# Optimization experiments

Measured on AMD Instinct MI355X. Metric: run time of the kernel, lower is better.

Reference implementation:

```python
import jax, jax.numpy as jnp
import numpy as np

N_NODES = 50000
EPS_NORM = 1e-12
EPS_ENT = 1e-8

def _l2norm(x):
    # torch.nn.functional.normalize: x / clamp(||x||, min=1e-12)
    n = jnp.sqrt(jnp.sum(x * x, axis=-1, keepdims=True))
    return x / jnp.maximum(n, EPS_NORM)

def _layer(hidden, src, dst, edge_type, multi_emb, proto_emb):
    # hidden: [N,H]; multi_emb: [R,P,H]; proto_emb: [P,H]
    inp_j = hidden[src]                          # [E,H] gather
    rel_basis = multi_emb[edge_type]             # [E,P,H] gather
    sims = jnp.einsum('eh,ph->ep', _l2norm(inp_j), _l2norm(proto_emb))  # cosine sim [E,P]
    proto_proba = jax.nn.softmax(sims, axis=1)   # [E,P]
    msg = jnp.einsum('ep,eph->eh', proto_proba, rel_basis)              # [E,H]
    ent = -jnp.sum(proto_proba * jnp.log(proto_proba + EPS_ENT), axis=1)  # [E]
    logits = -ent
    # scatter_softmax over destination index
    seg_max = jax.ops.segment_max(logits, dst, num_segments=N_NODES)
    ex = jnp.exp(logits - seg_max[dst])
    denom = jax.ops.segment_sum(ex, dst, num_segments=N_NODES)
    attn = ex / denom[dst]                       # [E]
    out = jax.ops.segment_sum(attn[:, None] * msg, dst, num_segments=N_NODES)  # [N,H]
    return out

def setup_inputs() -> dict:
    key = jax.random.key(0)
    ks = jax.random.split(key, 6)
    E = 800000
    H, R, P, L = 128, 18, 18, 3  # num_layers=4 -> 3 NBFCluttr layers
    edge_index = jax.random.randint(ks[0], (2, E), 0, N_NODES, dtype=jnp.int64) if jax.config.read('jax_enable_x64') else jax.random.randint(ks[0], (2, E), 0, N_NODES, dtype=jnp.int32)
    edge_type = jax.random.randint(ks[1], (E,), 0, R, dtype=edge_index.dtype)
    tail_indices = jax.random.randint(ks[2], (1024,), 0, N_NODES, dtype=edge_index.dtype)
    multi_embeddings = jax.random.uniform(ks[3], (L, R, P, H), dtype=jnp.float32)
    proto_embeddings = jax.random.uniform(ks[4], (L, P, H), dtype=jnp.float32)
    source_embedding = jax.random.uniform(ks[5], (H,), dtype=jnp.float32)
    return {"edge_index": edge_index, "edge_type": edge_type, "tail_indices": tail_indices,
            "multi_embeddings": multi_embeddings, "proto_embeddings": proto_embeddings,
            "source_embedding": source_embedding}

def reference(edge_index, edge_type, tail_indices, multi_embeddings, proto_embeddings, source_embedding):
    src, dst = edge_index[0], edge_index[1]
    H = source_embedding.shape[0]
    # boundary condition: source node gets source_embedding, rest zero
    hidden = jnp.zeros((N_NODES, H), dtype=source_embedding.dtype).at[0].set(source_embedding)
    L = multi_embeddings.shape[0]
    for l in range(L):  # small fixed loop over structurally distinct layers
        hidden = _layer(hidden, src, dst, edge_type, multi_embeddings[l], proto_embeddings[l])
    # apply_classifier, eval_mode=True, use_mlp_classifier=False -> cosine sims to last layer prototypes
    out_emb = hidden[tail_indices]               # [B,H]
    sims = jnp.einsum('nh,ph->np', _l2norm(out_emb), _l2norm(proto_embeddings[-1]))
    return sims  # gumbel_softmax_sample with eval_mode=True returns logits unchanged
```

## Files before the change

### kernel.cpp

```cpp
#include <hip/hip_runtime.h>
#include <hip/hip_bf16.h>


#define N_NODES 50000
#define H 128
#define P 18
#define RP 324
#define KPAD 352
#define K0PAD 64
#define ELLW 48
#define NPART 8
#define NODES_PER_PART 6250

typedef _Float16 half8 __attribute__((ext_vector_type(8)));
typedef _Float16 half4 __attribute__((ext_vector_type(4)));
typedef float floatx4 __attribute__((ext_vector_type(4)));

__global__ __launch_bounds__(256) void ell_kernel(const int* __restrict__ src,
                                                  const int* __restrict__ dst,
                                                  const int* __restrict__ etype,
                                                  unsigned* __restrict__ cur,
                                                  unsigned* __restrict__ ep, int E) {
  int part = blockIdx.x & (NPART - 1);
  int i = (blockIdx.x >> 3) * 256 + threadIdx.x;
  if (i >= E) return;
  int d = dst[i];
  int lo = part * NODES_PER_PART;
  if (d < lo || d >= lo + NODES_PER_PART) return;
  unsigned pos = atomicAdd(&cur[d], 1u);
  if (pos < ELLW)
    ep[(size_t)d * ELLW + pos] = (unsigned)src[i] | ((unsigned)etype[i] << 20);
}

__global__ __launch_bounds__(256) void prep_kernel(const float* __restrict__ proto,
                                                   const float* __restrict__ semb,
                                                   const float* __restrict__ multi,
                                                   float* __restrict__ pN,
                                                   _Float16* __restrict__ Btg,
                                                   _Float16* __restrict__ Btl0,
                                                   unsigned* __restrict__ cur) {
  int bid = blockIdx.x, tid = threadIdx.x;
  int gi = bid * 256 + tid;
  if (gi < N_NODES) cur[gi] = 0u;

  if (bid < 54) {
    if (tid < 64) {
      int row = bid, l = tid;
      float a = proto[row * H + l], b = proto[row * H + 64 + l];
      float ss = a * a + b * b;
      for (int m = 32; m > 0; m >>= 1) ss += __shfl_xor(ss, m, 64);
      float inv = 1.f / fmaxf(sqrtf(ss), 1e-12f);
      pN[row * H + l] = a * inv;
      pN[row * H + 64 + l] = b * inv;
    }
    return;
  }
  if (bid < 406) {
    int idx = (bid - 54) * 256 + tid;
    int l = idx / (H * KPAD), rem = idx - l * (H * KPAD);
    int h = rem / KPAD, k = rem - h * KPAD;
    const float* B = multi + (size_t)(l + 1) * RP * H;
    Btg[idx] = (k < RP) ? (_Float16)B[k * H + h] : (_Float16)0.f;
    return;
  }
  __shared__ float qs[P];
  if (tid < 64) {
    int l = tid;
    float s0 = semb[l], s1 = semb[l + 64];
    float ss = s0 * s0 + s1 * s1;
    float dot[P];
#pragma unroll
    for (int p = 0; p < P; p++) {
      float a = proto[p * H + l], b = proto[p * H + 64 + l];
      float rn = a * a + b * b;
      for (int m = 32; m > 0; m >>= 1) rn += __shfl_xor(rn, m, 64);
      float rinv = 1.f / fmaxf(sqrtf(rn), 1e-12f);
      dot[p] = (s0 * a + s1 * b) * rinv;
    }
    for (int m = 1; m <= 32; m <<= 1) {
      ss += __shfl_xor(ss, m, 64);
#pragma unroll
      for (int p = 0; p < P; p++) dot[p] += __shfl_xor(dot[p], m, 64);
    }
    float inv = 1.f / fmaxf(sqrtf(ss), 1e-12f);
    float sum = 0.f;
#pragma unroll
    for (int p = 0; p < P; p++) {
      dot[p] = __expf(dot[p] * inv - 1.f);
      sum += dot[p];
    }
    float isum = 1.f / sum, ent = 0.f;
#pragma unroll
    for (int p = 0; p < P; p++) {
      dot[p] *= isum;
      ent -= dot[p] * __logf(dot[p] + 1e-8f);
    }
    float w = __expf(-ent);
    if (l < P) qs[l] = w * dot[l];
  }
  __syncthreads();
  int idx2 = (bid - 406) * 256 + tid;
  if (idx2 >= H * K0PAD) return;
  int h = idx2 >> 6, k = idx2 & 63;
  float pr = 1.f / 18.f, ent = 0.f;
#pragma unroll
  for (int p = 0; p < P; p++) ent -= pr * __logf(pr + 1e-8f);
  float qc = __expf(-ent) * pr;
  float v = 0.f;
  if (k < P) {
#pragma unroll
    for (int p = 0; p < P; p++) v += qc * multi[(k * P + p) * H + h];
  } else if (k < 2 * P) {
    int r = k - P;
#pragma unroll
    for (int p = 0; p < P; p++) v += (qs[p] - qc) * multi[(r * P + p) * H + h];
  }
  Btl0[h * K0PAD + k] = (_Float16)v;
}

__global__ __launch_bounds__(256) void hist_kernel(const unsigned* __restrict__ ep,
                                                   const unsigned* __restrict__ cur,
                                                   _Float16* __restrict__ M, int n) {
  int wave = threadIdx.x >> 6, lane = threadIdx.x & 63;
  int nd = blockIdx.x * 4 + wave;
  if (nd >= n) return;
  int cnt = (int)cur[nd];
  if (cnt > ELLW) cnt = ELLW;
  bool a = lane < cnt;
  unsigned pk = a ? ep[(size_t)nd * ELLW + lane] : 0xFFFFFFFFu;
  int r = (int)(pk >> 20);
  unsigned long long zm = __ballot(a && (pk & 0xFFFFFu) == 0u);
  float creg = 0.f, creg0 = 0.f;
#pragma unroll
  for (int rr = 0; rr < P; rr++) {
    unsigned long long m = __ballot(a && (r == rr));
    if (lane == rr) {
      creg = (float)__popcll(m);
      creg0 = (float)__popcll(m & zm);
    }
  }
  int slx = (lane >= P && lane < 2 * P) ? lane - P : 0;
  float v0 = __shfl(creg0, slx, 64);
  float val = (lane < P) ? creg : ((lane < 2 * P) ? v0 : 0.f);
  M[(size_t)nd * K0PAD + lane] = (_Float16)val;
}

__global__ __launch_bounds__(256) void scatter_kernel(const unsigned* __restrict__ ep,
                                                      const unsigned* __restrict__ cur,
                                                      const _Float16* __restrict__ q,
                                                      const int* __restrict__ tl,
                                                      _Float16* __restrict__ M, int n) {
  __shared__ float sl[4][3 * RP];
  int wave = threadIdx.x >> 6, lane = threadIdx.x & 63;
  int t = blockIdx.x * 4 + wave;
  float* s0 = sl[wave];
  for (int i = lane; i < 3 * RP; i += 64) s0[i] = 0.f;
  int cnt = 0;
  size_t b = 0;
  if (t < n) {
    int nd = tl ? tl[t] : t;
    b = (size_t)nd * ELLW;
    cnt = (int)cur[nd];
    if (cnt > ELLW) cnt = ELLW;
  }
  unsigned eload = 0xFFFFFFFFu;
  if (t < n && lane < cnt) eload = ep[b + lane];
  int sub = lane / 18;
  int j = lane - sub * 18;
  bool act = (sub < 3) && (t < n);
  float* ms = s0 + (sub < 3 ? sub : 0) * RP;
  for (int base = 0; base < cnt; base += 24) {
    unsigned pk[8];
    float qv[8];
    bool av[8];
#pragma unroll
    for (int u = 0; u < 8; u++) {
      int e = base + sub + 3 * u;
      av[u] = act && (e < cnt);
      pk[u] = __shfl(eload, e & 63, 64);
      qv[u] = 0.f;
      if (av[u]) qv[u] = (float)q[(size_t)(pk[u] & 0xFFFFFu) * P + j];
    }
#pragma unroll
    for (int u = 0; u < 8; u++)
      if (av[u]) ms[(pk[u] >> 20) * P + j] += qv[u];
  }
  if (t < n) {
    for (int k = lane; k < RP; k += 64)
      M[(size_t)t * KPAD + k] = (_Float16)(s0[k] + s0[RP + k] + s0[2 * RP + k]);
    for (int k = RP + lane; k < KPAD; k += 64) M[(size_t)t * KPAD + k] = (_Float16)0.f;
  }
}

template <int MODE>
__global__ __launch_bounds__(256) void gemm_kernel(const _Float16* __restrict__ M,
                                                   const _Float16* __restrict__ Bt,
                                                   const float* __restrict__ pN,
                                                   void* __restrict__ out_ptr, int n,
                                                   int kpad) {
  __shared__ _Float16 smem_h[64 * 132];
  _Float16* As = smem_h;
  _Float16* Bs = smem_h + 2048;
  int tid = threadIdx.x;
  int wave = tid >> 6, lane = tid & 63;
  int m15 = lane & 15, quad = lane >> 4;
  int n0 = blockIdx.x * 64;
  floatx4 acc[4][2] = {};

  __shared__ _Float16 pns[4 * P * 36];
  for (int i = tid; i < 4 * P * 32; i += 256) {
    int s = i / (P * 32), r = i - s * (P * 32);
    int p = r >> 5, kk = r & 31;
    pns[s * (P * 36) + p * 36 + kk] = (_Float16)pN[p * H + s * 32 + kk];
  }

  for (int kt = 0; kt < (kpad >> 5); kt++) {
    int k0 = kt * 32;
    __syncthreads();
    {
      int row = tid >> 2, kc = (tid & 3) * 8;
      int gr = n0 + row;
      half8 v = {};
      if (gr < n) v = *(const half8*)(M + (size_t)gr * kpad + k0 + kc);
      *(half8*)(As + row * 32 + kc) = v;
    }
    {
      int col = tid >> 1, kc = (tid & 1) * 16;
      const _Float16* srcp = Bt + (size_t)col * kpad + k0 + kc;
      *(half8*)(Bs + col * 32 + kc) = *(const half8*)srcp;
      *(half8*)(Bs + col * 32 + kc + 8) = *(const half8*)(srcp + 8);
    }
    __syncthreads();
    half8 bfrag0 = *(const half8*)(Bs + (wave * 32 + m15) * 32 + quad * 8);
    half8 bfrag1 = *(const half8*)(Bs + (wave * 32 + 16 + m15) * 32 + quad * 8);
#pragma unroll
    for (int mt = 0; mt < 4; mt++) {
      half8 afrag = *(const half8*)(As + (mt * 16 + m15) * 32 + quad * 8);
      acc[mt][0] = __builtin_amdgcn_mfma_f32_16x16x32_f16(afrag, bfrag0, acc[mt][0], 0, 0, 0);
      acc[mt][1] = __builtin_amdgcn_mfma_f32_16x16x32_f16(afrag, bfrag1, acc[mt][1], 0, 0, 0);
    }
  }
  __syncthreads();
#pragma unroll
  for (int mt = 0; mt < 4; mt++)
#pragma unroll
    for (int c = 0; c < 2; c++)
#pragma unroll
      for (int reg = 0; reg < 4; reg++)
        smem_h[(mt * 16 + quad * 4 + reg) * 132 + wave * 32 + c * 16 + m15] =
            (_Float16)acc[mt][c][reg];
  __syncthreads();
  int node = tid >> 2, sub = tid & 3;
  int gnode = n0 + node;
  const _Float16* trow = smem_h + node * 132 + sub * 32;
  const _Float16* ps = pns + sub * (P * 36);
  float ss = 0.f;
  float dot[P];
#pragma unroll
  for (int p = 0; p < P; p++) dot[p] = 0.f;
#pragma unroll
  for (int k4 = 0; k4 < 8; k4++) {
    half4 yh = *(const half4*)(trow + k4 * 4);
    float y0 = (float)yh.x, y1 = (float)yh.y, y2 = (float)yh.z, y3 = (float)yh.w;
    ss += y0 * y0 + y1 * y1 + y2 * y2 + y3 * y3;
#pragma unroll
    for (int p = 0; p < P; p++) {
      half4 bh = *(const half4*)(ps + p * 36 + k4 * 4);
      dot[p] += y0 * (float)bh.x + y1 * (float)bh.y + y2 * (float)bh.z + y3 * (float)bh.w;
    }
  }
  for (int m = 1; m <= 2; m <<= 1) {
    ss += __shfl_xor(ss, m, 64);
#pragma unroll
    for (int p = 0; p < P; p++) dot[p] += __shfl_xor(dot[p], m, 64);
  }
  if (gnode < n) {
    float inv = 1.f / fmaxf(sqrtf(ss), 1e-12f);
    if (MODE == 1) {
      float* outp = (float*)out_ptr;
      for (int p = sub; p < P; p += 4) outp[(size_t)gnode * P + p] = dot[p] * inv;
    } else {
      float sum = 0.f;
#pragma unroll
      for (int p = 0; p < P; p++) {
        dot[p] = __expf(dot[p] * inv - 1.f);
        sum += dot[p];
      }
      float isum = 1.f / sum, ent = 0.f;
#pragma unroll
      for (int p = 0; p < P; p++) {
        dot[p] *= isum;
        ent -= dot[p] * __logf(dot[p] + 1e-8f);
      }
      float w = __expf(-ent);
      _Float16* qp = (_Float16*)out_ptr;
      for (int p = sub; p < P; p += 4) qp[(size_t)gnode * P + p] = (_Float16)(w * dot[p]);
    }
  }
}

extern "C" void kernel_launch(void* const* d_in, const int* in_sizes, int n_in,
                              void* d_out, int out_size, void* d_ws, size_t ws_size,
                              hipStream_t stream) {
  const int* eidx = (const int*)d_in[0];
  int E = in_sizes[0] / 2;
  const int* src = eidx;
  const int* dst = eidx + E;
  const int* etype = (const int*)d_in[1];
  const int* tails = (const int*)d_in[2];
  int T = in_sizes[2];
  const float* multi = (const float*)d_in[3];
  const float* proto = (const float*)d_in[4];
  const float* semb = (const float*)d_in[5];
  float* out = (float*)d_out;

  char* w = (char*)d_ws;
  auto alloc = [&](size_t bytes) {
    char* p = w;
    w += (bytes + 255) & ~(size_t)255;
    return p;
  };
  _Float16* q = (_Float16*)alloc((size_t)N_NODES * P * 2);
  float* pNs = (float*)alloc((size_t)3 * P * H * 4);
  _Float16* Mg = (_Float16*)alloc((size_t)N_NODES * KPAD * 2);
  _Float16* Btg = (_Float16*)alloc((size_t)2 * H * KPAD * 2);
  _Float16* Btl0 = (_Float16*)alloc((size_t)H * K0PAD * 2);
  unsigned* cur = (unsigned*)alloc((size_t)N_NODES * 4);
  unsigned* ep = (unsigned*)alloc((size_t)N_NODES * ELLW * 4);

  int eb = (E + 255) / 256;

  prep_kernel<<<438, 256, 0, stream>>>(proto, semb, multi, pNs, Btg, Btl0, cur);

  ell_kernel<<<eb * NPART, 256, 0, stream>>>(src, dst, etype, cur, ep, E);

  hist_kernel<<<(N_NODES + 3) / 4, 256, 0, stream>>>(ep, cur, Mg, N_NODES);
  gemm_kernel<0><<<(N_NODES + 63) / 64, 256, 0, stream>>>(Mg, Btl0, pNs + (size_t)1 * P * H, q,
                                                          N_NODES, K0PAD);

  scatter_kernel<<<(N_NODES + 3) / 4, 256, 0, stream>>>(ep, cur, q, nullptr, Mg, N_NODES);
  gemm_kernel<0><<<(N_NODES + 63) / 64, 256, 0, stream>>>(Mg, Btg, pNs + (size_t)2 * P * H, q,
                                                          N_NODES, KPAD);

  scatter_kernel<<<(T + 3) / 4, 256, 0, stream>>>(ep, cur, q, tails, Mg, T);
  gemm_kernel<1><<<(T + 63) / 64, 256, 0, stream>>>(Mg, Btg + (size_t)H * KPAD,
                                                    pNs + (size_t)2 * P * H, out, T, KPAD);
}
```

Before: 239.6 us.

## Fuse layer-0 histogram with its GEMM and prototype softmax into one kernel

Replaces the histogram kernel that wrote per-node relation counts to M, and the following layer-0 GEMM, with one kernel. The new kernel computes the hidden vector from the counts against the layer-0 basis held in shared memory, then the cosine similarity, softmax, entropy weight and q directly. This removes one launch and the round trip of the M matrix through global memory. In exchange each block reloads the basis and prototype tables into shared memory and does more shuffle reductions per node.

Result: slower. 368.2 us (+53.7%).

```diff
diff --git a/kernel.cpp b/kernel.cpp
--- a/kernel.cpp
+++ b/kernel.cpp
@@ -118,10 +118,22 @@
   Btl0[h * K0PAD + k] = (_Float16)v;
 }
 
-__global__ __launch_bounds__(256) void hist_kernel(const unsigned* __restrict__ ep,
-                                                   const unsigned* __restrict__ cur,
-                                                   _Float16* __restrict__ M, int n) {
-  int wave = threadIdx.x >> 6, lane = threadIdx.x & 63;
+__global__ __launch_bounds__(256) void histq_kernel(const unsigned* __restrict__ ep,
+                                                    const unsigned* __restrict__ cur,
+                                                    const _Float16* __restrict__ Btl0,
+                                                    const float* __restrict__ pN1,
+                                                    _Float16* __restrict__ q, int n) {
+  __shared__ float bt0t[2 * P * H];
+  __shared__ float pn1s[P * H];
+  int tid = threadIdx.x;
+  for (int i = tid; i < 2 * P * H; i += 256) {
+    int k = i >> 7, h = i & 127;
+    bt0t[i] = (float)Btl0[h * K0PAD + k];
+  }
+  for (int i = tid; i < P * H; i += 256) pn1s[i] = pN1[i];
+  __syncthreads();
+
+  int wave = tid >> 6, lane = tid & 63;
   int nd = blockIdx.x * 4 + wave;
   if (nd >= n) return;
   int cnt = (int)cur[nd];
@@ -139,10 +151,42 @@
       creg0 = (float)__popcll(m & zm);
     }
   }
-  int slx = (lane >= P && lane < 2 * P) ? lane - P : 0;
-  float v0 = __shfl(creg0, slx, 64);
-  float val = (lane < P) ? creg : ((lane < 2 * P) ? v0 : 0.f);
-  M[(size_t)nd * K0PAD + lane] = (_Float16)val;
+  float y0 = 0.f, y1 = 0.f;
+#pragma unroll
+  for (int rr = 0; rr < P; rr++) {
+    float ca = __shfl(creg, rr, 64);
+    float c0 = __shfl(creg0, rr, 64);
+    y0 += ca * bt0t[rr * H + lane] + c0 * bt0t[(P + rr) * H + lane];
+    y1 += ca * bt0t[rr * H + 64 + lane] + c0 * bt0t[(P + rr) * H + 64 + lane];
+  }
+  float ss = y0 * y0 + y1 * y1;
+  float dot[P];
+#pragma unroll
+  for (int p = 0; p < P; p++)
+    dot[p] = y0 * pn1s[p * H + lane] + y1 * pn1s[p * H + 64 + lane];
+  for (int m = 1; m <= 32; m <<= 1) {
+    ss += __shfl_xor(ss, m, 64);
+#pragma unroll
+    for (int p = 0; p < P; p++) dot[p] += __shfl_xor(dot[p], m, 64);
+  }
+  float inv = 1.f / fmaxf(sqrtf(ss), 1e-12f);
+  float sum = 0.f;
+#pragma unroll
+  for (int p = 0; p < P; p++) {
+    dot[p] = __expf(dot[p] * inv - 1.f);
+    sum += dot[p];
+  }
+  float isum = 1.f / sum, ent = 0.f;
+#pragma unroll
+  for (int p = 0; p < P; p++) {
+    dot[p] *= isum;
+    ent -= dot[p] * __logf(dot[p] + 1e-8f);
+  }
+  float w = __expf(-ent);
+  float outv = 0.f;
+#pragma unroll
+  for (int p = 0; p < P; p++) outv = (lane == p) ? w * dot[p] : outv;
+  if (lane < P) q[(size_t)nd * P + lane] = (_Float16)outv;
 }
 
 __global__ __launch_bounds__(256) void scatter_kernel(const unsigned* __restrict__ ep,
@@ -334,9 +378,8 @@
 
   ell_kernel<<<eb * NPART, 256, 0, stream>>>(src, dst, etype, cur, ep, E);
 
-  hist_kernel<<<(N_NODES + 3) / 4, 256, 0, stream>>>(ep, cur, Mg, N_NODES);
-  gemm_kernel<0><<<(N_NODES + 63) / 64, 256, 0, stream>>>(Mg, Btl0, pNs + (size_t)1 * P * H, q,
-                                                          N_NODES, K0PAD);
+  histq_kernel<<<(N_NODES + 3) / 4, 256, 0, stream>>>(ep, cur, Btl0,
+                                                      pNs + (size_t)1 * P * H, q, N_NODES);
 
   scatter_kernel<<<(N_NODES + 3) / 4, 256, 0, stream>>>(ep, cur, q, nullptr, Mg, N_NODES);
   gemm_kernel<0><<<(N_NODES + 63) / 64, 256, 0, stream>>>(Mg, Btg, pNs + (size_t)2 * P * H, q,
```
